# Kernel tuning notes

Measured on AMD Instinct MI355X. Metric: run time of the kernel, lower is better.

Reference implementation:

```python
import jax, jax.numpy as jnp
import numpy as np

B, INDIM, OUTDIM = 1024, 2048, 4096


def setup_inputs() -> dict:
    key = jax.random.key(0)
    kx, kw, kb = jax.random.split(key, 3)
    x = jax.random.normal(kx, (B, INDIM), dtype=jnp.float32)
    # nn.Linear(indim, outdim): weight [outdim, indim], bias [outdim]
    bound = 1.0 / np.sqrt(INDIM)
    W = jax.random.uniform(kw, (OUTDIM, INDIM), minval=-bound, maxval=bound, dtype=jnp.float32)
    b = jax.random.uniform(kb, (OUTDIM,), minval=-bound, maxval=bound, dtype=jnp.float32)
    return {"x": x, "W": W, "b": b}


def reference(x, W, b):
    # Faithful to torch: prototypes = weight.transpose(0,1).reshape(outdim, indim)
    # (a reflatten of W^T, not the original weight rows, since outdim != indim).
    protos = W.T.reshape(W.shape[0], W.shape[1])  # [outdim, indim]
    # -||x_i - p_j||^2 - b_j via GEMM identity (same math as broadcast subtract + norm^2)
    x_sq = jnp.sum(x * x, axis=1, keepdims=True)          # [B, 1]
    p_sq = jnp.sum(protos * protos, axis=1)[None, :]      # [1, outdim]
    xp = jnp.einsum('bd,od->bo', x, protos)               # [B, outdim]
    return -(x_sq - 2.0 * xp + p_sq) - b[None, :]
```

## Files before the change

### kernel.cpp

```cpp
#include <hip/hip_runtime.h>

#define IN_DIM  2048
#define OUT_DIM 4096

typedef float     f32x4 __attribute__((ext_vector_type(4)));
typedef long long llx2  __attribute__((ext_vector_type(2)));

__device__ __forceinline__ unsigned int pk4(float a, float b, float c, float d) {
    int v = __builtin_amdgcn_cvt_pk_fp8_f32(a, b, 0, false);
    v     = __builtin_amdgcn_cvt_pk_fp8_f32(c, d, v, true);
    return (unsigned int)v;
}

__device__ __forceinline__ void async16(const void* g, void* l) {
    __builtin_amdgcn_global_load_lds(
        (const __attribute__((address_space(1))) unsigned int*)g,
        (__attribute__((address_space(3))) unsigned int*)l,
        16, 0, 0);
}

__device__ __forceinline__ int gmem_of(int c) { return 2 * (c & 3) + (c >> 2); }

extern "C" __global__ __launch_bounds__(256) void transpose_w(
        const float* __restrict__ W, unsigned char* __restrict__ protos,
        float* __restrict__ psq) {
    __shared__ float tile[64][65];
    const int r  = blockIdx.z;
    const int c0 = blockIdx.x * 64;
    const int d0 = blockIdx.y * 64;
    const int t  = threadIdx.x;
    const int g  = t >> 4;
    const int cc = (t & 15) * 4;

    const float* Wp = W + (size_t)(r * IN_DIM + d0 + g) * IN_DIM + c0 + cc;
#pragma unroll
    for (int p = 0; p < 4; ++p) {
        const float4 v = *(const float4*)(Wp + (size_t)(16 * p) * IN_DIM);
        const int dl = g + 16 * p;
        tile[dl][cc]     = v.x;
        tile[dl][cc + 1] = v.y;
        tile[dl][cc + 2] = v.z;
        tile[dl][cc + 3] = v.w;
    }
    __syncthreads();

    const int c8 = t & 7;
    const int gm = gmem_of(c8);
#pragma unroll
    for (int p = 0; p < 2; ++p) {
        const int cr = (t >> 3) + 32 * p;
        float v[8];
        float ss = 0.f;
#pragma unroll
        for (int j = 0; j < 8; ++j) {
            v[j] = tile[8 * c8 + j][cr];
            ss += v[j] * v[j];
        }
        const int o = 2 * (c0 + cr) + r;
        uint2 pk;
        pk.x = pk4(16.f * v[0], 16.f * v[1], 16.f * v[2], 16.f * v[3]);
        pk.y = pk4(16.f * v[4], 16.f * v[5], 16.f * v[6], 16.f * v[7]);
        *(uint2*)(protos + (size_t)o * IN_DIM + d0 + gm * 8) = pk;
        ss += __shfl_xor(ss, 1);
        ss += __shfl_xor(ss, 2);
        ss += __shfl_xor(ss, 4);
        if (c8 == 0) atomicAdd(psq + o, ss);
    }
}

extern "C" __global__ __launch_bounds__(256) void xcast_xsq(
        const float* __restrict__ x,
        unsigned char* __restrict__ xb,
        float* __restrict__ x_sq) {
    __shared__ float red[4];
    const int b = blockIdx.x;
    const int t = threadIdx.x;
    const float* xp = x + (size_t)b * IN_DIM + t * 8;
    const float4 v0 = ((const float4*)xp)[0];
    const float4 v1 = ((const float4*)xp)[1];
    uint2 pk;
    pk.x = pk4(v0.x, v0.y, v0.z, v0.w);
    pk.y = pk4(v1.x, v1.y, v1.z, v1.w);
    *(uint2*)(xb + (size_t)b * IN_DIM + (t >> 3) * 64 + gmem_of(t & 7) * 8) = pk;

    float s = v0.x * v0.x + v0.y * v0.y + v0.z * v0.z + v0.w * v0.w
            + v1.x * v1.x + v1.y * v1.y + v1.z * v1.z + v1.w * v1.w;
#pragma unroll
    for (int off = 32; off > 0; off >>= 1) s += __shfl_down(s, off);
    const int lane = t & 63, w = t >> 6;
    if (lane == 0) red[w] = s;
    __syncthreads();
    if (t == 0) x_sq[b] = red[0] + red[1] + red[2] + red[3];
}

extern "C" __global__ __launch_bounds__(256) void gemm_epi(
        const unsigned char* __restrict__ A,
        const unsigned char* __restrict__ Bt,
        const float* __restrict__ x_sq,
        const float* __restrict__ psq,
        const float* __restrict__ bias,
        float* __restrict__ out) {
    __shared__ __align__(16) unsigned char lA[64 * 64];
    __shared__ __align__(16) unsigned char lB[64 * 64];

    const int lid = blockIdx.x;
    const int xcd = lid & 7;
    const int wi  = lid >> 3;
    const int nt  = xcd * 8 + (wi & 7);
    const int mt  = wi >> 3;
    const int m0 = mt * 64;
    const int n0 = nt * 64;

    const int t  = threadIdx.x;
    const int rS = t >> 2;
    const int pS = (t & 3) ^ ((rS >> 1) & 3);
    const unsigned char* gA = A  + (size_t)(m0 + rS) * IN_DIM + pS * 16;
    const unsigned char* gB = Bt + (size_t)(n0 + rS) * IN_DIM + pS * 16;
    unsigned char* lAd = lA + t * 16;
    unsigned char* lBd = lB + t * 16;

    const int wave = t >> 6;
    const int lane = t & 63;
    const int wm = (wave & 1) * 32;
    const int wn = (wave >> 1) * 32;
    const int ln = lane & 15;
    const int qd = lane >> 4;
    const int pf = qd ^ ((ln >> 1) & 3);

    f32x4 acc[2][2] = {};

    for (int k0 = 0; k0 < IN_DIM; k0 += 64) {
        async16(gA, lAd);
        async16(gB, lBd);
        gA += 64; gB += 64;
        __syncthreads();

        llx2 af[2], bf[2];
#pragma unroll
        for (int i = 0; i < 2; ++i)
            af[i] = *(const llx2*)(lA + (wm + i * 16 + ln) * 64 + pf * 16);
#pragma unroll
        for (int j = 0; j < 2; ++j)
            bf[j] = *(const llx2*)(lB + (wn + j * 16 + ln) * 64 + pf * 16);
#pragma unroll
        for (int kk = 0; kk < 2; ++kk)
#pragma unroll
            for (int i = 0; i < 2; ++i)
#pragma unroll
                for (int j = 0; j < 2; ++j)
                    acc[i][j] = __builtin_amdgcn_mfma_f32_16x16x32_fp8_fp8(
                                    af[i][kk], bf[j][kk], acc[i][j], 0, 0, 0);
        __syncthreads();
    }

    const int rowb = m0 + wm;
    const int colb = n0 + wn;
#pragma unroll
    for (int j = 0; j < 2; ++j) {
        const int col = colb + j * 16 + ln;
        const float pb = psq[col] + bias[col];
#pragma unroll
        for (int i = 0; i < 2; ++i) {
            const int row0 = rowb + i * 16 + qd * 4;
#pragma unroll
            for (int rr = 0; rr < 4; ++rr) {
                const int row = row0 + rr;
                out[(size_t)row * OUT_DIM + col] =
                    0.125f * acc[i][j][rr] - x_sq[row] - pb;
            }
        }
    }
}

extern "C" void kernel_launch(void* const* d_in, const int* in_sizes, int n_in,
                              void* d_out, int out_size, void* d_ws, size_t ws_size,
                              hipStream_t stream) {
    const float* x    = (const float*)d_in[0];
    const float* W    = (const float*)d_in[1];
    const float* bias = (const float*)d_in[2];
    float* out = (float*)d_out;

    char* ws = (char*)d_ws;
    unsigned char* protos = (unsigned char*)ws;
    unsigned char* xb     = (unsigned char*)(ws + (size_t)8 * 1024 * 1024);
    float* x_sq           = (float*)(ws + (size_t)10 * 1024 * 1024);
    float* psq            = (float*)(ws + (size_t)10 * 1024 * 1024 + 8192);

    hipMemsetAsync(psq, 0, OUT_DIM * sizeof(float), stream);
    transpose_w<<<dim3(32, 32, 2), 256, 0, stream>>>(W, protos, psq);
    xcast_xsq<<<dim3(1024), 256, 0, stream>>>(x, xb, x_sq);
    gemm_epi<<<dim3(1024), 256, 0, stream>>>(xb, protos, x_sq, psq, bias, out);
}
```

Baseline: 109.7 us.

## Split-K across waves in GEMM with 128-wide K steps; fuse psq zeroing into xcast

The GEMM now loads 128 K-bytes per iteration, so it runs 16 iterations with half as many barriers. The four waves split into two K halves, each wave covering all 64 rows and 32 columns, and the partial accumulators are reduced through LDS before the epilogue. LDS is reused for the reduction, the swizzle moves to an 8-chunk XOR, and launch bounds ask for 4 blocks per CU. The hipMemsetAsync for psq is dropped: xcast_xsq now zeroes psq and runs before transpose_w, which removes one launch at the cost of an extra LDS reduction and more registers.

```diff
diff --git a/kernel.cpp b/kernel.cpp
--- a/kernel.cpp
+++ b/kernel.cpp
@@ -71,10 +71,12 @@
 extern "C" __global__ __launch_bounds__(256) void xcast_xsq(
         const float* __restrict__ x,
         unsigned char* __restrict__ xb,
-        float* __restrict__ x_sq) {
+        float* __restrict__ x_sq,
+        float* __restrict__ psq) {
     __shared__ float red[4];
     const int b = blockIdx.x;
     const int t = threadIdx.x;
+    if (t < 4) psq[b * 4 + t] = 0.f;
     const float* xp = x + (size_t)b * IN_DIM + t * 8;
     const float4 v0 = ((const float4*)xp)[0];
     const float4 v1 = ((const float4*)xp)[1];
@@ -93,15 +95,16 @@
     if (t == 0) x_sq[b] = red[0] + red[1] + red[2] + red[3];
 }
 
-extern "C" __global__ __launch_bounds__(256) void gemm_epi(
+extern "C" __global__ __launch_bounds__(256, 4) void gemm_epi(
         const unsigned char* __restrict__ A,
         const unsigned char* __restrict__ Bt,
         const float* __restrict__ x_sq,
         const float* __restrict__ psq,
         const float* __restrict__ bias,
         float* __restrict__ out) {
-    __shared__ __align__(16) unsigned char lA[64 * 64];
-    __shared__ __align__(16) unsigned char lB[64 * 64];
+    __shared__ __align__(16) unsigned char smem[16384];
+    unsigned char* lA = smem;
+    unsigned char* lB = smem + 8192;
 
     const int lid = blockIdx.x;
     const int xcd = lid & 7;
@@ -111,41 +114,45 @@
     const int m0 = mt * 64;
     const int n0 = nt * 64;
 
-    const int t  = threadIdx.x;
-    const int rS = t >> 2;
-    const int pS = (t & 3) ^ ((rS >> 1) & 3);
-    const unsigned char* gA = A  + (size_t)(m0 + rS) * IN_DIM + pS * 16;
-    const unsigned char* gB = Bt + (size_t)(n0 + rS) * IN_DIM + pS * 16;
+    const int t = threadIdx.x;
+    const int rS = t >> 3;
+    const int pS = t & 7;
+    const int lS = pS ^ (rS & 7);
+    const size_t goff = (size_t)(lS >> 2) * 1024 + (lS & 3) * 16;
+    const unsigned char* gA0 = A  + (size_t)(m0 + rS) * IN_DIM + goff;
+    const unsigned char* gA1 = gA0 + (size_t)32 * IN_DIM;
+    const unsigned char* gB0 = Bt + (size_t)(n0 + rS) * IN_DIM + goff;
+    const unsigned char* gB1 = gB0 + (size_t)32 * IN_DIM;
     unsigned char* lAd = lA + t * 16;
     unsigned char* lBd = lB + t * 16;
 
     const int wave = t >> 6;
     const int lane = t & 63;
-    const int wm = (wave & 1) * 32;
-    const int wn = (wave >> 1) * 32;
+    const int kh = wave & 1;
+    const int nh = wave >> 1;
     const int ln = lane & 15;
     const int qd = lane >> 4;
-    const int pf = qd ^ ((ln >> 1) & 3);
-
-    f32x4 acc[2][2] = {};
-
-    for (int k0 = 0; k0 < IN_DIM; k0 += 64) {
-        async16(gA, lAd);
-        async16(gB, lBd);
-        gA += 64; gB += 64;
+    const int pr = (kh * 4 + qd) ^ (ln & 7);
+
+    f32x4 acc[4][2] = {};
+
+    for (int it = 0; it < 16; ++it) {
+        async16(gA0, lAd); async16(gA1, lAd + 4096);
+        async16(gB0, lBd); async16(gB1, lBd + 4096);
+        gA0 += 64; gA1 += 64; gB0 += 64; gB1 += 64;
         __syncthreads();
 
-        llx2 af[2], bf[2];
-#pragma unroll
-        for (int i = 0; i < 2; ++i)
-            af[i] = *(const llx2*)(lA + (wm + i * 16 + ln) * 64 + pf * 16);
+        llx2 af[4], bf[2];
+#pragma unroll
+        for (int i = 0; i < 4; ++i)
+            af[i] = *(const llx2*)(lA + (i * 16 + ln) * 128 + pr * 16);
 #pragma unroll
         for (int j = 0; j < 2; ++j)
-            bf[j] = *(const llx2*)(lB + (wn + j * 16 + ln) * 64 + pf * 16);
+            bf[j] = *(const llx2*)(lB + (nh * 32 + j * 16 + ln) * 128 + pr * 16);
 #pragma unroll
         for (int kk = 0; kk < 2; ++kk)
 #pragma unroll
-            for (int i = 0; i < 2; ++i)
+            for (int i = 0; i < 4; ++i)
 #pragma unroll
                 for (int j = 0; j < 2; ++j)
                     acc[i][j] = __builtin_amdgcn_mfma_f32_16x16x32_fp8_fp8(
@@ -153,20 +160,33 @@
         __syncthreads();
     }
 
-    const int rowb = m0 + wm;
-    const int colb = n0 + wn;
-#pragma unroll
-    for (int j = 0; j < 2; ++j) {
-        const int col = colb + j * 16 + ln;
-        const float pb = psq[col] + bias[col];
-#pragma unroll
-        for (int i = 0; i < 2; ++i) {
-            const int row0 = rowb + i * 16 + qd * 4;
-#pragma unroll
-            for (int rr = 0; rr < 4; ++rr) {
-                const int row = row0 + rr;
-                out[(size_t)row * OUT_DIM + col] =
-                    0.125f * acc[i][j][rr] - x_sq[row] - pb;
+    if (kh == 1) {
+#pragma unroll
+        for (int i = 0; i < 4; ++i)
+#pragma unroll
+            for (int j = 0; j < 2; ++j)
+                *(f32x4*)(smem + nh * 8192 + (i * 2 + j) * 1024 + lane * 16) =
+                    acc[i][j];
+    }
+    __syncthreads();
+    if (kh == 0) {
+        const int rowb = m0;
+        const int colb = n0 + nh * 32;
+#pragma unroll
+        for (int j = 0; j < 2; ++j) {
+            const int col = colb + j * 16 + ln;
+            const float pb = psq[col] + bias[col];
+#pragma unroll
+            for (int i = 0; i < 4; ++i) {
+                const f32x4 o4 = *(const f32x4*)(smem + nh * 8192 +
+                                                 (i * 2 + j) * 1024 + lane * 16);
+                const int row0 = rowb + i * 16 + qd * 4;
+#pragma unroll
+                for (int rr = 0; rr < 4; ++rr) {
+                    const int row = row0 + rr;
+                    out[(size_t)row * OUT_DIM + col] =
+                        0.125f * (acc[i][j][rr] + o4[rr]) - x_sq[row] - pb;
+                }
             }
         }
     }
@@ -186,8 +206,7 @@
     float* x_sq           = (float*)(ws + (size_t)10 * 1024 * 1024);
     float* psq            = (float*)(ws + (size_t)10 * 1024 * 1024 + 8192);
 
-    hipMemsetAsync(psq, 0, OUT_DIM * sizeof(float), stream);
+    xcast_xsq<<<dim3(1024), 256, 0, stream>>>(x, xb, x_sq, psq);
     transpose_w<<<dim3(32, 32, 2), 256, 0, stream>>>(W, protos, psq);
-    xcast_xsq<<<dim3(1024), 256, 0, stream>>>(x, xb, x_sq);
     gemm_epi<<<dim3(1024), 256, 0, stream>>>(xb, protos, x_sq, psq, bias, out);
 }
```

Result: no change. 109.1 us (-0.6%).
